# Kernel optimization log

Measured on AMD Instinct MI355X. Metric: run time of the kernel, lower is better.

Reference implementation:

```python
import jax, jax.numpy as jnp
import numpy as np

VOCAB = 32000
EMBED = 2048
MAX_DELTAS = 4
NUM_TOKENS = 8192


def setup_inputs() -> dict:
    key = jax.random.key(0)
    k1, k2, k3, k4 = jax.random.split(key, 4)
    x = jax.random.randint(k1, (NUM_TOKENS,), 0, VOCAB, dtype=jnp.int32)
    # per-token adapter index; -1 would mean "no adapter" (kernel skips). Here all in-range.
    indices = jax.random.randint(k2, (NUM_TOKENS,), 0, MAX_DELTAS, dtype=jnp.int32)
    weight = jax.random.normal(k3, (VOCAB, EMBED), dtype=jnp.float32)
    delta_weights = jax.random.normal(k4, (MAX_DELTAS, VOCAB, EMBED), dtype=jnp.float32)
    return {"x": x, "indices": indices, "weight": weight, "delta_weights": delta_weights}


def reference(x, indices, weight, delta_weights):
    # tp_size == 1: masked_input = x, no vocab-range masking, all_reduce is identity.
    # Base embedding gather: [T, D]
    base = weight[x]
    # apply_delta_embed: per-token gather from the selected adapter's delta table,
    # added in-place to the base embedding. indices < 0 => no delta.
    valid = indices >= 0
    safe_idx = jnp.where(valid, indices, 0)
    delta = delta_weights[safe_idx, x]  # [T, D] double gather
    out = base + jnp.where(valid[:, None], delta, jnp.zeros((), dtype=delta.dtype))
    return out
```

## Files before the change

### kernel.cpp

```cpp
#include <hip/hip_runtime.h>


#define EMBED 2048
#define VOCAB 32000
#define CHUNKS (EMBED / 4)

__global__ __launch_bounds__(256)
void VocabParallelEmbeddingWithDelta_28973849379098_kernel(
        const int* __restrict__ x,
        const int* __restrict__ indices,
        const float* __restrict__ weight,
        const float* __restrict__ delta_weights,
        float* __restrict__ out) {
    const int token = blockIdx.x;
    const int tok_id = x[token];
    const int adapter = indices[token];

    const float4* __restrict__ wrow =
        (const float4*)(weight + (size_t)tok_id * EMBED);
    float4* __restrict__ orow = (float4*)(out + (size_t)token * EMBED);

    if (adapter >= 0) {
        const float4* __restrict__ drow =
            (const float4*)(delta_weights +
                            ((size_t)adapter * VOCAB + (size_t)tok_id) * EMBED);
        #pragma unroll
        for (int i = 0; i < 2; ++i) {
            const int c = threadIdx.x + i * 256;
            float4 w = wrow[c];
            float4 d = drow[c];
            w.x += d.x; w.y += d.y; w.z += d.z; w.w += d.w;
            orow[c] = w;
        }
    } else {
        #pragma unroll
        for (int i = 0; i < 2; ++i) {
            const int c = threadIdx.x + i * 256;
            orow[c] = wrow[c];
        }
    }
}

extern "C" void kernel_launch(void* const* d_in, const int* in_sizes, int n_in,
                              void* d_out, int out_size, void* d_ws, size_t ws_size,
                              hipStream_t stream) {
    const int*   x             = (const int*)d_in[0];
    const int*   indices       = (const int*)d_in[1];
    const float* weight        = (const float*)d_in[2];
    const float* delta_weights = (const float*)d_in[3];
    float*       out           = (float*)d_out;

    const int num_tokens = in_sizes[0];

    VocabParallelEmbeddingWithDelta_28973849379098_kernel
        <<<num_tokens, 256, 0, stream>>>(x, indices, weight, delta_weights, out);
}
```

Measured before the change: 1.243 ms.

## Use persistent grid-stride blocks with index prefetch and nontemporal loads/stores

Replaces one block per token with a capped grid of 2048 persistent blocks that loop over tokens and prefetch the next token's id and adapter index. Delta rows are read, and output rows written, with nontemporal hints so streaming data does not pollute the cache, while base weight rows use normal loads. The aim is less launch and scheduling overhead and better cache behaviour for this bandwidth-bound gather. The trade-off is fewer blocks in flight, which could limit memory-level parallelism.

Result: no change. 1.236 ms (-0.5%).

```diff
diff --git a/kernel.cpp b/kernel.cpp
--- a/kernel.cpp
+++ b/kernel.cpp
@@ -3,41 +3,63 @@
 
 #define EMBED 2048
 #define VOCAB 32000
-#define CHUNKS (EMBED / 4)
+#define BLOCK 256
+#define MAXGRID 2048
 
-__global__ __launch_bounds__(256)
+typedef float f32x4 __attribute__((ext_vector_type(4)));
+
+__global__ __launch_bounds__(BLOCK)
 void VocabParallelEmbeddingWithDelta_28973849379098_kernel(
         const int* __restrict__ x,
         const int* __restrict__ indices,
         const float* __restrict__ weight,
         const float* __restrict__ delta_weights,
-        float* __restrict__ out) {
-    const int token = blockIdx.x;
-    const int tok_id = x[token];
-    const int adapter = indices[token];
+        float* __restrict__ out,
+        const int num_tokens) {
+    const int stride = gridDim.x;
+    int t = blockIdx.x;
+    if (t >= num_tokens) return;
 
-    const float4* __restrict__ wrow =
-        (const float4*)(weight + (size_t)tok_id * EMBED);
-    float4* __restrict__ orow = (float4*)(out + (size_t)token * EMBED);
+    int tok = x[t];
+    int ad  = indices[t];
 
-    if (adapter >= 0) {
-        const float4* __restrict__ drow =
-            (const float4*)(delta_weights +
-                            ((size_t)adapter * VOCAB + (size_t)tok_id) * EMBED);
-        #pragma unroll
-        for (int i = 0; i < 2; ++i) {
-            const int c = threadIdx.x + i * 256;
-            float4 w = wrow[c];
-            float4 d = drow[c];
-            w.x += d.x; w.y += d.y; w.z += d.z; w.w += d.w;
-            orow[c] = w;
+    for (;;) {
+        const int  tn       = t + stride;
+        const bool has_next = (tn < num_tokens);
+        int ntok = 0, nad = 0;
+        if (has_next) {
+            ntok = x[tn];
+            nad  = indices[tn];
         }
-    } else {
-        #pragma unroll
-        for (int i = 0; i < 2; ++i) {
-            const int c = threadIdx.x + i * 256;
-            orow[c] = wrow[c];
+
+        const f32x4* __restrict__ wrow =
+            (const f32x4*)(weight + (size_t)tok * EMBED);
+        f32x4* __restrict__ orow = (f32x4*)(out + (size_t)t * EMBED);
+
+        if (ad >= 0) {
+            const f32x4* __restrict__ drow =
+                (const f32x4*)(delta_weights +
+                               ((size_t)ad * VOCAB + (size_t)tok) * EMBED);
+            #pragma unroll
+            for (int i = 0; i < 2; ++i) {
+                const int c = threadIdx.x + i * BLOCK;
+                f32x4 w = wrow[c];
+                f32x4 d = __builtin_nontemporal_load(&drow[c]);
+                w += d;
+                __builtin_nontemporal_store(w, &orow[c]);
+            }
+        } else {
+            #pragma unroll
+            for (int i = 0; i < 2; ++i) {
+                const int c = threadIdx.x + i * BLOCK;
+                __builtin_nontemporal_store(wrow[c], &orow[c]);
+            }
         }
+
+        if (!has_next) break;
+        t   = tn;
+        tok = ntok;
+        ad  = nad;
     }
 }
 
@@ -51,7 +73,9 @@
     float*       out           = (float*)d_out;
 
     const int num_tokens = in_sizes[0];
+    const int grid = num_tokens < MAXGRID ? num_tokens : MAXGRID;
 
     VocabParallelEmbeddingWithDelta_28973849379098_kernel
-        <<<num_tokens, 256, 0, stream>>>(x, indices, weight, delta_weights, out);
+        <<<grid, BLOCK, 0, stream>>>(x, indices, weight, delta_weights, out,
+                                     num_tokens);
 }
```
